# Performance work log

Measured on AMD Instinct MI355X. Metric: run time of the kernel, lower is better.

Reference implementation:

```python
import jax, jax.numpy as jnp
import numpy as np

N, M = 120000, 32
VX, VY = 0.16, 0.16
X_OFF = VX / 2 + 0.0          # vx/2 + pc_range[0]
Y_OFF = VY / 2 + (-39.68)     # vy/2 + pc_range[1]
BN_EPS = 1e-3


def setup_inputs() -> dict:
    key = jax.random.key(0)
    k1, k2, k3, k4, k5 = jax.random.split(key, 5)
    features = jax.random.normal(k1, (N, M, 4), dtype=jnp.float32)
    num_points = jax.random.randint(k2, (N,), 1, M + 1)              # >=1 point per pillar
    cy = jax.random.randint(k3, (N, 1), 0, 496)
    cx = jax.random.randint(k4, (N, 1), 0, 432)
    zeros = jnp.zeros((N, 2), dtype=jnp.int32)
    coors = jnp.concatenate([zeros, cy, cx], axis=1)                 # (N,4): [b, z, y, x]
    W = jax.random.normal(k5, (63, 9), dtype=jnp.float32) * 0.1      # Linear(9->63), no bias
    gamma = jnp.ones((63,), jnp.float32)
    beta = jnp.zeros((63,), jnp.float32)
    running_mean = jnp.zeros((63,), jnp.float32)
    running_var = jnp.ones((63,), jnp.float32)
    return {"features": features, "num_points": num_points, "coors": coors,
            "W": W, "gamma": gamma, "beta": beta,
            "running_mean": running_mean, "running_var": running_var}


def reference(features, num_points, coors, W, gamma, beta, running_mean, running_var):
    dt = features.dtype
    npf = num_points.astype(dt)[:, None, None]                        # (N,1,1)
    # distance to pillar centroid (xyz mean over points)
    voxels_mean = features[:, :, :3].sum(axis=1, keepdims=True) / npf
    centroid_dist = features[:, :, :3] - voxels_mean                  # (N,M,3)
    # offset from pillar base center (detached in the original)
    fxy = jax.lax.stop_gradient(features[:, :, :2])
    cx = fxy[:, :, 0] - (coors[:, 3].astype(dt)[:, None] * VX + X_OFF)
    cy = fxy[:, :, 1] - (coors[:, 2].astype(dt)[:, None] * VY + Y_OFF)
    base_center = jnp.stack([cx, cy], axis=-1)                        # (N,M,2)
    feats = jnp.concatenate([features, centroid_dist, base_center], axis=-1)  # (N,M,9)
    # zero out padded points
    mask = (jnp.arange(feats.shape[1])[None, :] < num_points[:, None]).astype(dt)[:, :, None]
    feats = feats * mask
    # PFNLayer (last layer, mode='max'): linear -> BN (eval stats) -> relu -> max over points
    x = jnp.einsum('nmc,uc->nmu', feats, W)                           # (N,M,63)
    inv = gamma / jnp.sqrt(running_var + BN_EPS)
    x = x * inv + (beta - running_mean * inv)
    x = jax.nn.relu(x)
    x_max = x.max(axis=1)                                             # (N,63)
    return jnp.concatenate([x_max, num_points.astype(dt)[:, None]], axis=-1)  # (N,64)
```

## Files before the change

kernel.cpp:

```cpp
#include <hip/hip_runtime.h>
#include <hip/hip_bf16.h>

typedef unsigned int u32;
typedef __attribute__((ext_vector_type(8))) short bf16x8;
typedef __attribute__((ext_vector_type(16))) float f32x16;
typedef __attribute__((ext_vector_type(4))) u32 u32x4;


#define XOFF (0.08f)
#define YOFF (0.08f - 39.68f)

#define SWZ_ADD(s, imm)                                                        \
    s += __builtin_bit_cast(float, __builtin_amdgcn_ds_swizzle(                \
             __builtin_bit_cast(int, s), imm))

__device__ __forceinline__ u32 f2bf_bits(float f) {
    union { float f; u32 u; } v; v.f = f;
    u32 u = v.u;
    u += 0x7fffu + ((u >> 16) & 1u);
    return u >> 16;
}
__device__ __forceinline__ short bf1(float f) { return (short)f2bf_bits(f); }

__device__ __forceinline__ u32 pk2(float lo, float hi) {
    __hip_bfloat162 h = __float22bfloat162_rn(make_float2(lo, hi));
    union { __hip_bfloat162 h; u32 u; } v; v.h = h;
    return v.u;
}

__device__ __forceinline__ float vmax16(const f32x16 v) {
    float m = fmaxf(fmaxf(v[0], v[1]), v[2]);
    m = fmaxf(fmaxf(m, v[3]), v[4]);
    m = fmaxf(fmaxf(m, v[5]), v[6]);
    m = fmaxf(fmaxf(m, v[7]), v[8]);
    m = fmaxf(fmaxf(m, v[9]), v[10]);
    m = fmaxf(fmaxf(m, v[11]), v[12]);
    m = fmaxf(fmaxf(m, v[13]), v[14]);
    return fmaxf(m, v[15]);
}

__device__ __forceinline__ void frontend(const float4 q, const int npts,
                                         const int2 cc, const int m,
                                         const int half,
                                         bf16x8& aA, bf16x8& aB)
{
    float sx = q.x, sy = q.y, sz = q.z;
    SWZ_ADD(sx, 0x041F); SWZ_ADD(sy, 0x041F); SWZ_ADD(sz, 0x041F);
    SWZ_ADD(sx, 0x081F); SWZ_ADD(sy, 0x081F); SWZ_ADD(sz, 0x081F);
    SWZ_ADD(sx, 0x101F); SWZ_ADD(sy, 0x101F); SWZ_ADD(sz, 0x101F);
    SWZ_ADD(sx, 0x201F); SWZ_ADD(sy, 0x201F); SWZ_ADD(sz, 0x201F);
    SWZ_ADD(sx, 0x401F); SWZ_ADD(sy, 0x401F); SWZ_ADD(sz, 0x401F);

    const float rnp = __builtin_amdgcn_rcpf((float)npts);
    const float mx = sx * rnp, my = sy * rnp, mz = sz * rnp;
    const float cxo = (float)cc.y * 0.16f + XOFF;
    const float cyo = (float)cc.x * 0.16f + YOFF;

    u32 p0 = pk2(q.x, q.y);
    u32 p1 = pk2(q.z, q.w);
    u32 p2 = pk2(q.x - mx, q.y - my);
    u32 p3 = pk2(q.z - mz, q.x - cxo);
    if (m >= npts) { p0 = 0; p1 = 0; p2 = 0; p3 = 0; }
    const u32 p4 = pk2((m < npts) ? q.y - cyo : 0.0f, 1.0f);

    const u32 x0 = __shfl_xor(p0, 32);
    const u32 x1 = __shfl_xor(p1, 32);
    const u32 x2 = __shfl_xor(p2, 32);
    const u32 x3 = __shfl_xor(p3, 32);
    const u32 x4 = __shfl_xor(p4, 32);

    u32x4 adw, bdw;
    adw[0] = half ? x4 : p0;  adw[1] = half ? 0u : p1;
    adw[2] = half ? 0u : p2;  adw[3] = half ? 0u : p3;
    bdw[0] = half ? p4 : x0;  bdw[1] = half ? 0u : x1;
    bdw[2] = half ? 0u : x2;  bdw[3] = half ? 0u : x3;
    aA = __builtin_bit_cast(bf16x8, adw);
    aB = __builtin_bit_cast(bf16x8, bdw);
}

__device__ __forceinline__ void backend(const bf16x8 aA, const bf16x8 aB,
                                        const bf16x8 b0, const bf16x8 b1,
                                        const f32x16 zacc, const int half,
                                        const int lane, const float npf,
                                        const int pairIdx, const int n_pairs,
                                        const int n_total,
                                        float* __restrict__ out)
{
    const f32x16 cA0 = __builtin_amdgcn_mfma_f32_32x32x16_bf16(aA, b0, zacc, 0, 0, 0);
    const f32x16 cA1 = __builtin_amdgcn_mfma_f32_32x32x16_bf16(aA, b1, zacc, 0, 0, 0);
    const float tA0 = vmax16(cA0);
    const float tA1 = vmax16(cA1);
    const f32x16 cB0 = __builtin_amdgcn_mfma_f32_32x32x16_bf16(aB, b0, zacc, 0, 0, 0);
    const f32x16 cB1 = __builtin_amdgcn_mfma_f32_32x32x16_bf16(aB, b1, zacc, 0, 0, 0);
    const float tB0 = vmax16(cB0);
    const float tB1 = vmax16(cB1);

    const float keepA = half ? tA1 : tA0, sendA = half ? tA0 : tA1;
    const float keepB = half ? tB1 : tB0, sendB = half ? tB0 : tB1;
    float vA = fmaxf(fmaxf(keepA, __shfl_xor(sendA, 32)), 0.0f);
    float vB = fmaxf(fmaxf(keepB, __shfl_xor(sendB, 32)), 0.0f);

    const float npo = __shfl_xor(npf, 32);
    if (lane == 63) { vA = npo; vB = npf; }

    if (pairIdx < n_pairs) {
        const int nA = pairIdx * 2;
        out[nA * 64 + lane] = vA;
        if (nA + 1 < n_total) out[(nA + 1) * 64 + lane] = vB;
    }
}

__global__ __launch_bounds__(256, 4)
void pfn_mfma(const float* __restrict__ features,
              const int* __restrict__ num_points,
              const int* __restrict__ coors,
              const float* __restrict__ W,
              const float* __restrict__ gamma,
              const float* __restrict__ beta,
              const float* __restrict__ rmean,
              const float* __restrict__ rvar,
              float* __restrict__ out,
              int n_total)
{
    const int lane = threadIdx.x & 63;
    const int wid  = threadIdx.x >> 6;
    const int half = lane >> 5;
    const int m    = lane & 31;
    const int waves_total = gridDim.x * 4;
    const int gwave = blockIdx.x * 4 + wid;

    const int c0 = m, c1 = 32 + m;
    const float inv0   = gamma[c0] / sqrtf(rvar[c0] + 1e-3f);
    const float shift0 = beta[c0] - rmean[c0] * inv0;
    float inv1 = 0.0f, shift1 = 0.0f;
    if (c1 < 63) {
        inv1   = gamma[c1] / sqrtf(rvar[c1] + 1e-3f);
        shift1 = beta[c1] - rmean[c1] * inv1;
    }

    bf16x8 b0, b1;
#pragma unroll
    for (int j = 0; j < 8; ++j) {
        const int k = half * 8 + j;
        float w0v = 0.0f, w1v = 0.0f;
        if (k < 9)       { w0v = W[c0 * 9 + k] * inv0;
                           w1v = (c1 < 63) ? W[c1 * 9 + k] * inv1 : 0.0f; }
        else if (k == 9) { w0v = shift0; w1v = shift1; }
        b0[j] = bf1(w0v);
        b1[j] = bf1(w1v);
    }

    const f32x16 zacc = {};
    const float4* featv = reinterpret_cast<const float4*>(features);
    const int n_pairs = (n_total + 1) >> 1;
    const int stride  = waves_total * 2;
    const int iters   = (n_pairs + stride - 1) / stride;

    auto load_pair = [&](int pr, float4& q, int& np, int2& cc) {
        int nh = min(pr, n_pairs - 1) * 2 + half;
        nh = min(nh, n_total - 1);
        np = num_points[nh];
        cc = *reinterpret_cast<const int2*>(coors + nh * 4 + 2);
        q  = featv[nh * 32 + m];
    };

    int pa = gwave;
    float4 qa, qb; int na_, nb_; int2 ca, cb;
    load_pair(pa, qa, na_, ca);
    load_pair(pa + waves_total, qb, nb_, cb);

    for (int it = 0; it < iters; ++it) {
        float4 qan, qbn; int nan_, nbn_; int2 can, cbn;
        load_pair(pa + stride, qan, nan_, can);
        load_pair(pa + stride + waves_total, qbn, nbn_, cbn);

        bf16x8 aA1, aB1, aA2, aB2;
        frontend(qa, na_, ca, m, half, aA1, aB1);
        frontend(qb, nb_, cb, m, half, aA2, aB2);

        backend(aA1, aB1, b0, b1, zacc, half, lane, (float)na_,
                pa,               n_pairs, n_total, out);
        backend(aA2, aB2, b0, b1, zacc, half, lane, (float)nb_,
                pa + waves_total, n_pairs, n_total, out);

        pa += stride;
        qa = qan; na_ = nan_; ca = can;
        qb = qbn; nb_ = nbn_; cb = cbn;
    }
}

extern "C" void kernel_launch(void* const* d_in, const int* in_sizes, int n_in,
                              void* d_out, int out_size, void* d_ws, size_t ws_size,
                              hipStream_t stream) {
    const float* features   = (const float*)d_in[0];
    const int*   num_points = (const int*)d_in[1];
    const int*   coors      = (const int*)d_in[2];
    const float* W          = (const float*)d_in[3];
    const float* gamma      = (const float*)d_in[4];
    const float* beta       = (const float*)d_in[5];
    const float* rmean      = (const float*)d_in[6];
    const float* rvar       = (const float*)d_in[7];
    float* out              = (float*)d_out;

    const int n_total = in_sizes[1];

    const int blocks = 2048;
    pfn_mfma<<<blocks, 256, 0, stream>>>(features, num_points, coors, W,
                                         gamma, beta, rmean, rvar, out, n_total);
}
```

Baseline: 126.8 us.

## Use DPP row reductions and redundant per-half loads to drop cross-half shuffles

Replaces four of the five ds_swizzle reduction steps for the per-pillar xyz sums with DPP row operations: xor1, xor2, half-mirror and mirror. Only the final 16-lane exchange still uses ds_swizzle. Each half-wave now loads both pillars of a pair itself, so the MFMA A fragments are built locally and the cross-half __shfl_xor exchanges of packed features and point counts go away. The cost is twice as many feature, num_points and coors load instructions per wave, although DRAM traffic should be unchanged because the duplicates should hit in cache. It also adds more live registers.

```diff
diff --git a/kernel.cpp b/kernel.cpp
--- a/kernel.cpp
+++ b/kernel.cpp
@@ -13,6 +13,17 @@
 #define SWZ_ADD(s, imm)                                                        \
     s += __builtin_bit_cast(float, __builtin_amdgcn_ds_swizzle(                \
              __builtin_bit_cast(int, s), imm))
+
+template <int CTRL>
+__device__ __forceinline__ float dpp_add(float s) {
+    int t = __builtin_amdgcn_update_dpp(0, __builtin_bit_cast(int, s),
+                                        CTRL, 0xF, 0xF, true);
+    return s + __builtin_bit_cast(float, t);
+}
+#define DPP_XOR1  0xB1
+#define DPP_XOR2  0x4E
+#define DPP_HMIRR 0x141
+#define DPP_MIRR  0x140
 
 __device__ __forceinline__ u32 f2bf_bits(float f) {
     union { float f; u32 u; } v; v.f = f;
@@ -39,49 +50,43 @@
     return fmaxf(m, v[15]);
 }
 
-__device__ __forceinline__ void frontend(const float4 q, const int npts,
-                                         const int2 cc, const int m,
-                                         const int half,
-                                         bf16x8& aA, bf16x8& aB)
+__device__ __forceinline__ bf16x8 build_frag(const float4 q, const int npts,
+                                             const int2 cc, const int m,
+                                             const int half)
 {
     float sx = q.x, sy = q.y, sz = q.z;
-    SWZ_ADD(sx, 0x041F); SWZ_ADD(sy, 0x041F); SWZ_ADD(sz, 0x041F);
-    SWZ_ADD(sx, 0x081F); SWZ_ADD(sy, 0x081F); SWZ_ADD(sz, 0x081F);
-    SWZ_ADD(sx, 0x101F); SWZ_ADD(sy, 0x101F); SWZ_ADD(sz, 0x101F);
-    SWZ_ADD(sx, 0x201F); SWZ_ADD(sy, 0x201F); SWZ_ADD(sz, 0x201F);
-    SWZ_ADD(sx, 0x401F); SWZ_ADD(sy, 0x401F); SWZ_ADD(sz, 0x401F);
+    sx = dpp_add<DPP_XOR1>(sx);  sy = dpp_add<DPP_XOR1>(sy);  sz = dpp_add<DPP_XOR1>(sz);
+    sx = dpp_add<DPP_XOR2>(sx);  sy = dpp_add<DPP_XOR2>(sy);  sz = dpp_add<DPP_XOR2>(sz);
+    sx = dpp_add<DPP_HMIRR>(sx); sy = dpp_add<DPP_HMIRR>(sy); sz = dpp_add<DPP_HMIRR>(sz);
+    sx = dpp_add<DPP_MIRR>(sx);  sy = dpp_add<DPP_MIRR>(sy);  sz = dpp_add<DPP_MIRR>(sz);
+    SWZ_ADD(sx, 0x401F);         SWZ_ADD(sy, 0x401F);         SWZ_ADD(sz, 0x401F);
 
     const float rnp = __builtin_amdgcn_rcpf((float)npts);
     const float mx = sx * rnp, my = sy * rnp, mz = sz * rnp;
     const float cxo = (float)cc.y * 0.16f + XOFF;
     const float cyo = (float)cc.x * 0.16f + YOFF;
+    const bool  v   = (m < npts);
 
     u32 p0 = pk2(q.x, q.y);
     u32 p1 = pk2(q.z, q.w);
     u32 p2 = pk2(q.x - mx, q.y - my);
     u32 p3 = pk2(q.z - mz, q.x - cxo);
-    if (m >= npts) { p0 = 0; p1 = 0; p2 = 0; p3 = 0; }
-    const u32 p4 = pk2((m < npts) ? q.y - cyo : 0.0f, 1.0f);
-
-    const u32 x0 = __shfl_xor(p0, 32);
-    const u32 x1 = __shfl_xor(p1, 32);
-    const u32 x2 = __shfl_xor(p2, 32);
-    const u32 x3 = __shfl_xor(p3, 32);
-    const u32 x4 = __shfl_xor(p4, 32);
-
-    u32x4 adw, bdw;
-    adw[0] = half ? x4 : p0;  adw[1] = half ? 0u : p1;
-    adw[2] = half ? 0u : p2;  adw[3] = half ? 0u : p3;
-    bdw[0] = half ? p4 : x0;  bdw[1] = half ? 0u : x1;
-    bdw[2] = half ? 0u : x2;  bdw[3] = half ? 0u : x3;
-    aA = __builtin_bit_cast(bf16x8, adw);
-    aB = __builtin_bit_cast(bf16x8, bdw);
+    if (!v) { p0 = 0; p1 = 0; p2 = 0; p3 = 0; }
+    const u32 p4 = pk2(v ? q.y - cyo : 0.0f, 1.0f);
+
+    u32x4 w;
+    w[0] = half ? p4 : p0;
+    w[1] = half ? 0u : p1;
+    w[2] = half ? 0u : p2;
+    w[3] = half ? 0u : p3;
+    return __builtin_bit_cast(bf16x8, w);
 }
 
 __device__ __forceinline__ void backend(const bf16x8 aA, const bf16x8 aB,
                                         const bf16x8 b0, const bf16x8 b1,
                                         const f32x16 zacc, const int half,
-                                        const int lane, const float npf,
+                                        const int lane,
+                                        const float npAf, const float npBf,
                                         const int pairIdx, const int n_pairs,
                                         const int n_total,
                                         float* __restrict__ out)
@@ -100,8 +105,7 @@
     float vA = fmaxf(fmaxf(keepA, __shfl_xor(sendA, 32)), 0.0f);
     float vB = fmaxf(fmaxf(keepB, __shfl_xor(sendB, 32)), 0.0f);
 
-    const float npo = __shfl_xor(npf, 32);
-    if (lane == 63) { vA = npo; vB = npf; }
+    if (lane == 63) { vA = npAf; vB = npBf; }
 
     if (pairIdx < n_pairs) {
         const int nA = pairIdx * 2;
@@ -156,36 +160,46 @@
     const int stride  = waves_total * 2;
     const int iters   = (n_pairs + stride - 1) / stride;
 
-    auto load_pair = [&](int pr, float4& q, int& np, int2& cc) {
-        int nh = min(pr, n_pairs - 1) * 2 + half;
-        nh = min(nh, n_total - 1);
-        np = num_points[nh];
-        cc = *reinterpret_cast<const int2*>(coors + nh * 4 + 2);
-        q  = featv[nh * 32 + m];
+    auto load_pair = [&](int pr, float4& qA, float4& qB,
+                         int& npA, int& npB, int2& cA, int2& cB) {
+        const int base = min(pr, n_pairs - 1) * 2;
+        const int nA = base;
+        const int nB = min(base + 1, n_total - 1);
+        npA = num_points[nA];
+        npB = num_points[nB];
+        cA  = *reinterpret_cast<const int2*>(coors + nA * 4 + 2);
+        cB  = *reinterpret_cast<const int2*>(coors + nB * 4 + 2);
+        qA  = featv[nA * 32 + m];
+        qB  = featv[nB * 32 + m];
     };
 
     int pa = gwave;
-    float4 qa, qb; int na_, nb_; int2 ca, cb;
-    load_pair(pa, qa, na_, ca);
-    load_pair(pa + waves_total, qb, nb_, cb);
+    float4 qa1, qb1, qa2, qb2;
+    int na1, nb1, na2, nb2;
+    int2 ca1, cb1, ca2, cb2;
+    load_pair(pa,               qa1, qb1, na1, nb1, ca1, cb1);
+    load_pair(pa + waves_total, qa2, qb2, na2, nb2, ca2, cb2);
 
     for (int it = 0; it < iters; ++it) {
-        float4 qan, qbn; int nan_, nbn_; int2 can, cbn;
-        load_pair(pa + stride, qan, nan_, can);
-        load_pair(pa + stride + waves_total, qbn, nbn_, cbn);
-
-        bf16x8 aA1, aB1, aA2, aB2;
-        frontend(qa, na_, ca, m, half, aA1, aB1);
-        frontend(qb, nb_, cb, m, half, aA2, aB2);
-
-        backend(aA1, aB1, b0, b1, zacc, half, lane, (float)na_,
+        float4 qa1n, qb1n, qa2n, qb2n;
+        int na1n, nb1n, na2n, nb2n;
+        int2 ca1n, cb1n, ca2n, cb2n;
+        load_pair(pa + stride,               qa1n, qb1n, na1n, nb1n, ca1n, cb1n);
+        load_pair(pa + stride + waves_total, qa2n, qb2n, na2n, nb2n, ca2n, cb2n);
+
+        const bf16x8 aA1 = build_frag(qa1, na1, ca1, m, half);
+        const bf16x8 aB1 = build_frag(qb1, nb1, cb1, m, half);
+        const bf16x8 aA2 = build_frag(qa2, na2, ca2, m, half);
+        const bf16x8 aB2 = build_frag(qb2, nb2, cb2, m, half);
+
+        backend(aA1, aB1, b0, b1, zacc, half, lane, (float)na1, (float)nb1,
                 pa,               n_pairs, n_total, out);
-        backend(aA2, aB2, b0, b1, zacc, half, lane, (float)nb_,
+        backend(aA2, aB2, b0, b1, zacc, half, lane, (float)na2, (float)nb2,
                 pa + waves_total, n_pairs, n_total, out);
 
         pa += stride;
-        qa = qan; na_ = nan_; ca = can;
-        qb = qbn; nb_ = nbn_; cb = cbn;
+        qa1 = qa1n; qb1 = qb1n; na1 = na1n; nb1 = nb1n; ca1 = ca1n; cb1 = cb1n;
+        qa2 = qa2n; qb2 = qb2n; na2 = na2n; nb2 = nb2n; ca2 = ca2n; cb2 = cb2n;
     }
 }
 
```

Result: slower. 130.0 us (+2.5%).
